# Kernel optimization log

Measured on AMD Instinct MI355X. Metric: run time of the kernel, lower is better.

Reference implementation:

```python
import jax, jax.numpy as jnp
import numpy as np

B, T, D_MODEL, D_STATE = 4, 4096, 1024, 256


def setup_inputs() -> dict:
    key = jax.random.key(0)
    ks = jax.random.split(key, 6)
    return {
        "x": jax.random.normal(ks[0], (B, T, D_MODEL), dtype=jnp.float32),
        "state": jnp.zeros((B, D_STATE), dtype=jnp.float32),
        "W_in": jax.random.normal(ks[1], (D_MODEL, D_STATE), dtype=jnp.float32) / np.sqrt(D_MODEL),
        "b_in": jnp.zeros((D_STATE,), dtype=jnp.float32),
        "lambda_param": jax.random.normal(ks[2], (D_STATE,), dtype=jnp.float32),
        "gamma_param": jax.random.normal(ks[3], (D_STATE,), dtype=jnp.float32),
        "W_out": jax.random.normal(ks[4], (D_STATE, D_MODEL), dtype=jnp.float32) / np.sqrt(D_STATE),
        "b_out": jnp.zeros((D_MODEL,), dtype=jnp.float32),
    }


def reference(x, state, W_in, b_in, lambda_param, gamma_param, W_out, b_out):
    # u: [B, T, d_state]
    u = jnp.einsum("btd,ds->bts", x, W_in) + b_in
    decay = jax.nn.sigmoid(lambda_param)          # [d_state]
    gu = gamma_param * u                          # [B, T, d_state]

    # linear recurrence h_t = decay * h_{t-1} + gu_t via associative scan over T
    # elements: (a, b) representing h -> a*h + b; combine: (a2*a1, a2*b1 + b2)
    a = jnp.broadcast_to(decay, gu.shape)         # [B, T, d_state]

    def combine(l, r):
        a1, b1 = l
        a2, b2 = r
        return (a2 * a1, a2 * b1 + b2)

    A, Bc = jax.lax.associative_scan(combine, (a, gu), axis=1)
    h = A * state[:, None, :] + Bc                # [B, T, d_state]

    y = jnp.einsum("bts,sd->btd", h, W_out) + b_out
    return y, h[:, -1, :]
```

## Files before the change

### kernel.cpp

```cpp
#include <hip/hip_runtime.h>
#include <hip/hip_bf16.h>
#include <math.h>

#define BB 4
#define TT 4096
#define DM 1024
#define DS 256
#define MROWS (BB*TT)

#define LCH 32
#define NCH (TT/LCH)

#define BM 128

typedef __attribute__((ext_vector_type(8))) _Float16 half8v;
typedef __attribute__((ext_vector_type(2))) _Float16 half2v;
typedef __attribute__((ext_vector_type(4))) float float4v;

__device__ __forceinline__ float sigmoidf_dev(float x) {
    return 1.0f / (1.0f + expf(-x));
}

__device__ __forceinline__ half2v cvt2_rtz(float a, float b) {
    auto r = __builtin_amdgcn_cvt_pkrtz(a, b);
    union { decltype(r) i; half2v o; } cv;
    cv.i = r;
    return cv.o;
}

__device__ __forceinline__ void gload16(const void* g, void* l) {
    __builtin_amdgcn_global_load_lds(
        (const __attribute__((address_space(1))) void*)g,
        (__attribute__((address_space(3))) void*)l, 16, 0, 0);
}

__global__ __launch_bounds__(256) void cvt_weights(
    const float* __restrict__ W1, _Float16* __restrict__ T1,
    const float* __restrict__ W2, _Float16* __restrict__ T2)
{
    const int half = blockIdx.x >> 10;
    int idx = (blockIdx.x & 1023) * 256 + threadIdx.x;
    const float* W = half ? W2 : W1;
    _Float16* T = half ? T2 : T1;
    const int K = half ? DS : DM;
    const int N = half ? DM : DS;
    int n = idx / K, k = idx - n * K;
    T[idx] = (_Float16)W[(size_t)k * N + n];
}

__global__ __launch_bounds__(256) void gemm1_fused(
    const float* __restrict__ x, const _Float16* __restrict__ Bt,
    float* __restrict__ gu,
    const float* __restrict__ bias, const float* __restrict__ scale,
    const float* __restrict__ lam, float* __restrict__ csum)
{
    __shared__ char smem[40960];
    constexpr int K = DM;
    constexpr int BN = 64, BK = 32, NF = 2, WCOLS = 32;

    const int nwg = gridDim.x;
    const int bid = blockIdx.x;
    const int wgid = (bid & 7) * (nwg >> 3) + (bid >> 3);
    const int GN = DS / BN;
    const int bm = wgid / GN;
    const int bn = wgid - bm * GN;

    const int tid  = threadIdx.x;
    const int lane = tid & 63;
    const int wv   = tid >> 6;
    const int wr   = wv >> 1;
    const int wc   = wv & 1;
    const int lrow = lane & 15;
    const int q16  = lane >> 4;

    const int NT = K / BK;
    float4v acc[4][NF] = {};

#define STAGE1(T, Q)                                                              \
    do {                                                                          \
        const int k0_ = (T) * BK;                                                 \
        _Pragma("unroll")                                                         \
        for (int p = 0; p < 4; p++) {                                             \
            int c = tid + p * 256, r = c >> 3, chp = c & 7;                       \
            const float* g = x + (size_t)(bm * BM + r) * K + k0_                  \
                               + ((chp ^ (r & 7)) << 2);                          \
            gload16(g, smem + (Q) * 16384 + c * 16);                              \
        }                                                                         \
        {                                                                         \
            int c = tid, r = c >> 2, chp = c & 3;                                 \
            const _Float16* g = Bt + (size_t)(bn * BN + r) * K + k0_              \
                                   + ((chp ^ ((r >> 1) & 3)) << 3);               \
            gload16(g, smem + 32768 + (Q) * 4096 + c * 16);                       \
        }                                                                         \
    } while (0)

    STAGE1(0, 0);
    __syncthreads();

    for (int t = 0; t < NT; ++t) {
        const int Q = t & 1;
        if (t + 1 < NT) STAGE1(t + 1, Q ^ 1);

        union { half2v h2[4]; half8v h8; } a[4];
        half8v b[NF];
#pragma unroll
        for (int i = 0; i < 4; i++) {
            int row = wr * 64 + i * 16 + lrow;
            const char* ab = smem + Q * 16384 + row * 128;
            int s = row & 7;
            float4 fa = *(const float4*)(ab + (((2 * q16)     ^ s) << 4));
            float4 fb = *(const float4*)(ab + (((2 * q16 + 1) ^ s) << 4));
            a[i].h2[0] = cvt2_rtz(fa.x, fa.y);
            a[i].h2[1] = cvt2_rtz(fa.z, fa.w);
            a[i].h2[2] = cvt2_rtz(fb.x, fb.y);
            a[i].h2[3] = cvt2_rtz(fb.z, fb.w);
        }
#pragma unroll
        for (int j = 0; j < NF; j++) {
            int row = wc * WCOLS + j * 16 + lrow;
            b[j] = *(const half8v*)(smem + 32768 + Q * 4096 +
                                    ((row * 4 + (q16 ^ ((row >> 1) & 3))) << 4));
        }

#pragma unroll
        for (int i = 0; i < 4; i++)
#pragma unroll
            for (int j = 0; j < NF; j++)
                acc[i][j] = __builtin_amdgcn_mfma_f32_16x16x32_f16(a[i].h8, b[j], acc[i][j], 0, 0, 0);

        __syncthreads();
    }

    float* gul = (float*)smem;
#pragma unroll
    for (int j = 0; j < NF; j++) {
        int col = bn * BN + wc * WCOLS + j * 16 + lrow;
        float bi = bias[col];
        float sc = scale[col];
#pragma unroll
        for (int i = 0; i < 4; i++) {
            int r0 = bm * BM + wr * 64 + i * 16 + q16 * 4;
#pragma unroll
            for (int reg = 0; reg < 4; reg++) {
                float v = (acc[i][j][reg] + bi) * sc;
                gu[(size_t)(r0 + reg) * DS + col] = v;
                int lr = wr * 64 + i * 16 + q16 * 4 + reg;
                int lc = wc * WCOLS + j * 16 + lrow;
                gul[lr * 68 + lc] = v;
            }
        }
    }

    __syncthreads();
    const int lc = tid >> 6;
    const int ch = tid & 63;
    const int gcol = bn * BN + ch;
    const float d = sigmoidf_dev(lam[gcol]);
    float h = 0.0f;
#pragma unroll
    for (int rr = 0; rr < LCH; rr++)
        h = fmaf(d, h, gul[(lc * LCH + rr) * 68 + ch]);
    const int row0 = bm * BM;
    const int b    = row0 >> 12;
    const int gch  = ((row0 & 4095) >> 5) + lc;
    csum[((size_t)b * NCH + gch) * DS + gcol] = h;
#undef STAGE1
}

__global__ __launch_bounds__(256) void gemm2_f16(
    const _Float16* __restrict__ A, const _Float16* __restrict__ Bt,
    float* __restrict__ C, const float* __restrict__ bias)
{
    constexpr int BN = 128, BK = 64, NF = 4, WCOLS = 64;
    constexpr int K = DS;
    constexpr int ABYTES = BM * BK * 2;
    constexpr int BUFB = ABYTES + BN * BK * 2;
    __shared__ char smem[2 * BUFB];

    const int nwg = gridDim.x;
    const int bid = blockIdx.x;
    const int wgid = (bid & 7) * (nwg >> 3) + (bid >> 3);
    const int GN = DM / BN;
    const int bm = wgid / GN;
    const int bn = wgid - bm * GN;

    const int tid  = threadIdx.x;
    const int lane = tid & 63;
    const int wv   = tid >> 6;
    const int wr   = wv >> 1;
    const int wc   = wv & 1;
    const int lrow = lane & 15;
    const int q16  = lane >> 4;

    const int NT = K / BK;
    float4v acc[4][NF] = {};

#define STAGE2(T, Q)                                                              \
    do {                                                                          \
        const int k0_ = (T) * BK;                                                 \
        char* base_ = smem + (Q) * BUFB;                                          \
        _Pragma("unroll")                                                         \
        for (int p = 0; p < 4; p++) {                                             \
            int c = tid + p * 256, r = c >> 3, chp = c & 7;                       \
            const _Float16* g = A + (size_t)(bm * BM + r) * K + k0_               \
                                  + ((chp ^ (r & 7)) << 3);                       \
            gload16(g, base_ + c * 16);                                           \
        }                                                                         \
        _Pragma("unroll")                                                         \
        for (int p = 0; p < 4; p++) {                                             \
            int c = tid + p * 256, r = c >> 3, chp = c & 7;                       \
            const _Float16* g = Bt + (size_t)(bn * BN + r) * K + k0_              \
                                   + ((chp ^ (r & 7)) << 3);                      \
            gload16(g, base_ + ABYTES + c * 16);                                  \
        }                                                                         \
    } while (0)

    STAGE2(0, 0);
    __syncthreads();

    for (int t = 0; t < NT; ++t) {
        const int Q = t & 1;
        if (t + 1 < NT) STAGE2(t + 1, Q ^ 1);

        char* const rb = smem + Q * BUFB;
        half8v a[4][2], b[NF][2];
#pragma unroll
        for (int i = 0; i < 4; i++) {
            int row = wr * 64 + i * 16 + lrow;
#pragma unroll
            for (int ss = 0; ss < 2; ss++) {
                int ch = ss * 4 + q16;
                a[i][ss] = *(const half8v*)(rb + ((row * 8 + (ch ^ (row & 7))) << 4));
            }
        }
#pragma unroll
        for (int j = 0; j < NF; j++) {
            int row = wc * WCOLS + j * 16 + lrow;
#pragma unroll
            for (int ss = 0; ss < 2; ss++) {
                int ch = ss * 4 + q16;
                b[j][ss] = *(const half8v*)(rb + ABYTES + ((row * 8 + (ch ^ (row & 7))) << 4));
            }
        }

#pragma unroll
        for (int ss = 0; ss < 2; ss++)
#pragma unroll
            for (int i = 0; i < 4; i++)
#pragma unroll
                for (int j = 0; j < NF; j++)
                    acc[i][j] = __builtin_amdgcn_mfma_f32_16x16x32_f16(a[i][ss], b[j][ss], acc[i][j], 0, 0, 0);

        __syncthreads();
    }

#pragma unroll
    for (int j = 0; j < NF; j++) {
        int col = bn * BN + wc * WCOLS + j * 16 + lrow;
        float bi = bias[col];
#pragma unroll
        for (int i = 0; i < 4; i++) {
            int r0 = bm * BM + wr * 64 + i * 16 + q16 * 4;
#pragma unroll
            for (int reg = 0; reg < 4; reg++)
                C[(size_t)(r0 + reg) * DM + col] = acc[i][j][reg] + bi;
        }
    }
#undef STAGE2
}

__global__ __launch_bounds__(256) void carry_scan(
    const float* __restrict__ csum, const float* __restrict__ state,
    const float* __restrict__ lam, float* __restrict__ carry, float* __restrict__ hlast)
{
    const int s = threadIdx.x;
    const int b = blockIdx.x;
    const float d = sigmoidf_dev(lam[s]);
    float dL = d;
#pragma unroll
    for (int i = 0; i < 5; i++) dL *= dL;
    float H = state[(size_t)b * DS + s];
#pragma unroll 8
    for (int k = 0; k < NCH; k++) {
        carry[((size_t)b * NCH + k) * DS + s] = H;
        H = fmaf(dL, H, csum[((size_t)b * NCH + k) * DS + s]);
    }
    hlast[(size_t)b * DS + s] = H;
}

__global__ __launch_bounds__(256) void scan_final(
    const float* __restrict__ gu, const float* __restrict__ lam,
    const float* __restrict__ carry, _Float16* __restrict__ hf)
{
    const int s = threadIdx.x;
    const int chunk = blockIdx.x;
    const int b = blockIdx.y;
    const float d = sigmoidf_dev(lam[s]);
    const size_t base = ((size_t)b * TT + (size_t)chunk * LCH) * DS + s;
    const float* p = gu + base;
    _Float16* ph = hf + base;
    float h = carry[((size_t)b * NCH + chunk) * DS + s];
#pragma unroll
    for (int t = 0; t < LCH; t++) {
        h = fmaf(d, h, p[(size_t)t * DS]);
        ph[(size_t)t * DS] = (_Float16)h;
    }
}

extern "C" void kernel_launch(void* const* d_in, const int* in_sizes, int n_in,
                              void* d_out, int out_size, void* d_ws, size_t ws_size,
                              hipStream_t stream) {
    const float* x     = (const float*)d_in[0];
    const float* state = (const float*)d_in[1];
    const float* W_in  = (const float*)d_in[2];
    const float* b_in  = (const float*)d_in[3];
    const float* lam   = (const float*)d_in[4];
    const float* gamma = (const float*)d_in[5];
    const float* W_out = (const float*)d_in[6];
    const float* b_out = (const float*)d_in[7];

    float* y     = (float*)d_out;
    float* hlast = y + (size_t)MROWS * DM;

    char* ws = (char*)d_ws;
    const size_t MB = 1024 * 1024;
    float*     gu    = (float*)(ws);
    float*     csum  = (float*)(ws + 16 * MB);
    float*     carry = (float*)(ws + 16 * MB + 512 * 1024);
    _Float16*  hf    = (_Float16*)(ws + 17 * MB);
    _Float16*  w1t   = (_Float16*)(ws + 25 * MB);
    _Float16*  w2t   = (_Float16*)(ws + 25 * MB + 512 * 1024);

    cvt_weights<<<dim3(2048), dim3(256), 0, stream>>>(W_in, w1t, W_out, w2t);

    gemm1_fused<<<dim3((MROWS / BM) * (DS / 64)), dim3(256), 0, stream>>>(
        x, w1t, gu, b_in, gamma, lam, csum);

    carry_scan<<<dim3(BB), dim3(256), 0, stream>>>(csum, state, lam, carry, hlast);
    scan_final<<<dim3(NCH, BB), dim3(256), 0, stream>>>(gu, lam, carry, hf);

    gemm2_f16<<<dim3((MROWS / BM) * (DM / 128)), dim3(256), 0, stream>>>(
        hf, w2t, y, b_out);
}
```

Before: 75.11 us.

## Convert A to fp16 on staging, double BK, store gu as fp16

```diff
diff --git a/kernel.cpp b/kernel.cpp
--- a/kernel.cpp
+++ b/kernel.cpp
@@ -50,13 +50,14 @@
 
 __global__ __launch_bounds__(256) void gemm1_fused(
     const float* __restrict__ x, const _Float16* __restrict__ Bt,
-    float* __restrict__ gu,
+    _Float16* __restrict__ gu,
     const float* __restrict__ bias, const float* __restrict__ scale,
     const float* __restrict__ lam, float* __restrict__ csum)
 {
-    __shared__ char smem[40960];
+    __shared__ char smem[49152];
     constexpr int K = DM;
-    constexpr int BN = 64, BK = 32, NF = 2, WCOLS = 32;
+    constexpr int BN = 64, BK = 64, NF = 2, WCOLS = 32;
+    constexpr int NT = K / BK;
 
     const int nwg = gridDim.x;
     const int bid = blockIdx.x;
@@ -73,61 +74,86 @@
     const int lrow = lane & 15;
     const int q16  = lane >> 4;
 
-    const int NT = K / BK;
     float4v acc[4][NF] = {};
-
-#define STAGE1(T, Q)                                                              \
+    float4 areg[8];
+
+    const int arow = tid >> 1;
+    const int acol = (tid & 1) * 32;
+    const int acb  = (tid & 1) * 4;
+
+#define LOADREG_A(T)                                                              \
     do {                                                                          \
-        const int k0_ = (T) * BK;                                                 \
-        _Pragma("unroll")                                                         \
-        for (int p = 0; p < 4; p++) {                                             \
-            int c = tid + p * 256, r = c >> 3, chp = c & 7;                       \
-            const float* g = x + (size_t)(bm * BM + r) * K + k0_                  \
-                               + ((chp ^ (r & 7)) << 2);                          \
-            gload16(g, smem + (Q) * 16384 + c * 16);                              \
-        }                                                                         \
-        {                                                                         \
-            int c = tid, r = c >> 2, chp = c & 3;                                 \
-            const _Float16* g = Bt + (size_t)(bn * BN + r) * K + k0_              \
-                                   + ((chp ^ ((r >> 1) & 3)) << 3);               \
-            gload16(g, smem + 32768 + (Q) * 4096 + c * 16);                       \
+        const float* g_ = x + (size_t)(bm * BM + arow) * K + (T) * BK + acol;     \
+        _Pragma("unroll")                                                         \
+        for (int p = 0; p < 8; p++) areg[p] = *(const float4*)(g_ + 4 * p);       \
+    } while (0)
+
+#define WRITE_A(Q)                                                                \
+    do {                                                                          \
+        char* base_ = smem + (Q) * 16384 + arow * 128;                            \
+        _Pragma("unroll")                                                         \
+        for (int ci = 0; ci < 4; ci++) {                                          \
+            union { half2v h2[4]; half8v h8; } u_;                                \
+            u_.h2[0] = cvt2_rtz(areg[2 * ci].x,     areg[2 * ci].y);              \
+            u_.h2[1] = cvt2_rtz(areg[2 * ci].z,     areg[2 * ci].w);              \
+            u_.h2[2] = cvt2_rtz(areg[2 * ci + 1].x, areg[2 * ci + 1].y);          \
+            u_.h2[3] = cvt2_rtz(areg[2 * ci + 1].z, areg[2 * ci + 1].w);          \
+            *(half8v*)(base_ + (((acb + ci) ^ (arow & 7)) << 4)) = u_.h8;         \
         }                                                                         \
     } while (0)
 
-    STAGE1(0, 0);
+#define STAGE_B(T, Q)                                                             \
+    do {                                                                          \
+        _Pragma("unroll")                                                         \
+        for (int p = 0; p < 2; p++) {                                             \
+            int c = tid + p * 256, r = c >> 3, chp = c & 7;                       \
+            const _Float16* g_ = Bt + (size_t)(bn * BN + r) * K + (T) * BK        \
+                                    + ((chp ^ (r & 7)) << 3);                     \
+            gload16(g_, smem + 32768 + (Q) * 8192 + c * 16);                      \
+        }                                                                         \
+    } while (0)
+
+    LOADREG_A(0);
+    STAGE_B(0, 0);
+    WRITE_A(0);
     __syncthreads();
 
     for (int t = 0; t < NT; ++t) {
         const int Q = t & 1;
-        if (t + 1 < NT) STAGE1(t + 1, Q ^ 1);
-
-        union { half2v h2[4]; half8v h8; } a[4];
-        half8v b[NF];
+        if (t + 1 < NT) {
+            STAGE_B(t + 1, Q ^ 1);
+            LOADREG_A(t + 1);
+        }
+
+        half8v a[4][2], b[NF][2];
 #pragma unroll
         for (int i = 0; i < 4; i++) {
             int row = wr * 64 + i * 16 + lrow;
-            const char* ab = smem + Q * 16384 + row * 128;
-            int s = row & 7;
-            float4 fa = *(const float4*)(ab + (((2 * q16)     ^ s) << 4));
-            float4 fb = *(const float4*)(ab + (((2 * q16 + 1) ^ s) << 4));
-            a[i].h2[0] = cvt2_rtz(fa.x, fa.y);
-            a[i].h2[1] = cvt2_rtz(fa.z, fa.w);
-            a[i].h2[2] = cvt2_rtz(fb.x, fb.y);
-            a[i].h2[3] = cvt2_rtz(fb.z, fb.w);
+#pragma unroll
+            for (int ss = 0; ss < 2; ss++) {
+                int ch = (ss * 4 + q16) ^ (row & 7);
+                a[i][ss] = *(const half8v*)(smem + Q * 16384 + row * 128 + ch * 16);
+            }
         }
 #pragma unroll
         for (int j = 0; j < NF; j++) {
             int row = wc * WCOLS + j * 16 + lrow;
-            b[j] = *(const half8v*)(smem + 32768 + Q * 4096 +
-                                    ((row * 4 + (q16 ^ ((row >> 1) & 3))) << 4));
-        }
-
-#pragma unroll
-        for (int i = 0; i < 4; i++)
-#pragma unroll
-            for (int j = 0; j < NF; j++)
-                acc[i][j] = __builtin_amdgcn_mfma_f32_16x16x32_f16(a[i].h8, b[j], acc[i][j], 0, 0, 0);
-
+#pragma unroll
+            for (int ss = 0; ss < 2; ss++) {
+                int ch = (ss * 4 + q16) ^ (row & 7);
+                b[j][ss] = *(const half8v*)(smem + 32768 + Q * 8192 + row * 128 + ch * 16);
+            }
+        }
+
+#pragma unroll
+        for (int ss = 0; ss < 2; ss++)
+#pragma unroll
+            for (int i = 0; i < 4; i++)
+#pragma unroll
+                for (int j = 0; j < NF; j++)
+                    acc[i][j] = __builtin_amdgcn_mfma_f32_16x16x32_f16(a[i][ss], b[j][ss], acc[i][j], 0, 0, 0);
+
+        if (t + 1 < NT) WRITE_A(Q ^ 1);
         __syncthreads();
     }
 
@@ -143,7 +169,7 @@
 #pragma unroll
             for (int reg = 0; reg < 4; reg++) {
                 float v = (acc[i][j][reg] + bi) * sc;
-                gu[(size_t)(r0 + reg) * DS + col] = v;
+                gu[(size_t)(r0 + reg) * DS + col] = (_Float16)v;
                 int lr = wr * 64 + i * 16 + q16 * 4 + reg;
                 int lc = wc * WCOLS + j * 16 + lrow;
                 gul[lr * 68 + lc] = v;
@@ -164,7 +190,9 @@
     const int b    = row0 >> 12;
     const int gch  = ((row0 & 4095) >> 5) + lc;
     csum[((size_t)b * NCH + gch) * DS + gcol] = h;
-#undef STAGE1
+#undef LOADREG_A
+#undef WRITE_A
+#undef STAGE_B
 }
 
 __global__ __launch_bounds__(256) void gemm2_f16(
@@ -289,7 +317,7 @@
 }
 
 __global__ __launch_bounds__(256) void scan_final(
-    const float* __restrict__ gu, const float* __restrict__ lam,
+    const _Float16* __restrict__ gu, const float* __restrict__ lam,
     const float* __restrict__ carry, _Float16* __restrict__ hf)
 {
     const int s = threadIdx.x;
@@ -297,12 +325,12 @@
     const int b = blockIdx.y;
     const float d = sigmoidf_dev(lam[s]);
     const size_t base = ((size_t)b * TT + (size_t)chunk * LCH) * DS + s;
-    const float* p = gu + base;
+    const _Float16* p = gu + base;
     _Float16* ph = hf + base;
     float h = carry[((size_t)b * NCH + chunk) * DS + s];
 #pragma unroll
     for (int t = 0; t < LCH; t++) {
-        h = fmaf(d, h, p[(size_t)t * DS]);
+        h = fmaf(d, h, (float)p[(size_t)t * DS]);
         ph[(size_t)t * DS] = (_Float16)h;
     }
 }
@@ -324,12 +352,12 @@
 
     char* ws = (char*)d_ws;
     const size_t MB = 1024 * 1024;
-    float*     gu    = (float*)(ws);
-    float*     csum  = (float*)(ws + 16 * MB);
-    float*     carry = (float*)(ws + 16 * MB + 512 * 1024);
-    _Float16*  hf    = (_Float16*)(ws + 17 * MB);
-    _Float16*  w1t   = (_Float16*)(ws + 25 * MB);
-    _Float16*  w2t   = (_Float16*)(ws + 25 * MB + 512 * 1024);
+    _Float16*  gu    = (_Float16*)(ws);
+    float*     csum  = (float*)(ws + 8 * MB);
+    float*     carry = (float*)(ws + 8 * MB + 512 * 1024);
+    _Float16*  hf    = (_Float16*)(ws + 9 * MB);
+    _Float16*  w1t   = (_Float16*)(ws + 17 * MB);
+    _Float16*  w2t   = (_Float16*)(ws + 17 * MB + 512 * 1024);
 
     cvt_weights<<<dim3(2048), dim3(256), 0, stream>>>(W_in, w1t, W_out, w2t);
 
```

After: 88.77 us. +18.2%, slower.
